# Performance work log

Measured on AMD Instinct MI355X. Metric: run time of the kernel, lower is better.

The kernel has to match this reference:

```python
import jax, jax.numpy as jnp
import numpy as np

# rho in the continualEP repo is the hard sigmoid: clamp to [0, 1]
def rho(x):
    return jnp.clip(x, 0.0, 1.0)

B = 16384
N0, N1, N2, ND = 10, 256, 256, 784  # size_tab = [N0, N1, N2, ND]; ns = 3
T_STEPS = 60


def _linear_init(key, out_dim, in_dim):
    s = 1.0 / np.sqrt(in_dim)
    return jax.random.uniform(key, (out_dim, in_dim), minval=-s, maxval=s, dtype=jnp.float32)


def setup_inputs() -> dict:
    key = jax.random.key(0)
    ks = jax.random.split(key, 8)
    data = jax.random.uniform(ks[0], (B, ND), dtype=jnp.float32)  # MNIST-like in [0,1]
    s0 = jnp.zeros((B, N0), jnp.float32)
    s1 = jnp.zeros((B, N1), jnp.float32)
    s2 = jnp.zeros((B, N2), jnp.float32)
    # w[0]: Linear(N1 -> N0, bias); w[1]: Linear(N0 -> N1, no bias), tied init W1 = W0^T
    W0 = _linear_init(ks[1], N0, N1)
    b0 = jax.random.uniform(ks[2], (N0,), minval=-1.0/np.sqrt(N1), maxval=1.0/np.sqrt(N1), dtype=jnp.float32)
    W1 = W0.T  # transpose-tied initialization (angle=0 branch)
    # w[2]: Linear(N2 -> N1, bias); w[3]: Linear(N1 -> N2, no bias), tied init W3 = W2^T
    W2 = _linear_init(ks[3], N1, N2)
    b2 = jax.random.uniform(ks[4], (N1,), minval=-1.0/np.sqrt(N2), maxval=1.0/np.sqrt(N2), dtype=jnp.float32)
    W3 = W2.T
    # w[4]: Linear(ND -> N2, bias)
    W4 = _linear_init(ks[5], N2, ND)
    b4 = jax.random.uniform(ks[6], (N2,), minval=-1.0/np.sqrt(ND), maxval=1.0/np.sqrt(ND), dtype=jnp.float32)
    return {"data": data, "s0": s0, "s1": s1, "s2": s2,
            "W0": W0, "b0": b0, "W1": W1, "W2": W2, "b2": b2,
            "W3": W3, "W4": W4, "b4": b4, "T": T_STEPS}


def reference(data, s0, s1, s2, W0, b0, W1, W2, b2, W3, W4, b4, T):
    """VFdisc.forward(method='nograd', beta=0): T sequential stepper() calls.

    stepper (dt=1):
      ds0 = -s0 + rho(W0 @ s1 + b0)
      ds1 = -s1 + rho(W2 @ s2 + b2 + W1 @ s0)
      ds2 = -s2 + rho(W4 @ data + b4 + W3 @ s1)
      s[i] <- s[i] + ds[i]   (all ds use the pre-update state)
    """
    # data drive is constant across steps; precompute it once
    drive = data @ W4.T + b4  # [B, N2]

    def step(carry, _):
        c0, c1, c2 = carry
        n0 = c0 + (-c0 + rho(c1 @ W0.T + b0))
        n1 = c1 + (-c1 + rho(c2 @ W2.T + b2 + c0 @ W1.T))
        n2 = c2 + (-c2 + rho(drive + c1 @ W3.T))
        return (n0, n1, n2), None

    (s0, s1, s2), _ = jax.lax.scan(step, (s0, s1, s2), None, length=T)
    return (s0, s1, s2)
```

## Files before the change

### kernel.cpp

```cpp
#include <hip/hip_runtime.h>

typedef __attribute__((ext_vector_type(8)))  short s8b;
typedef __attribute__((ext_vector_type(16))) float v16f;
typedef __attribute__((ext_vector_type(4)))  float v4f;
typedef __attribute__((ext_vector_type(4)))  unsigned int u32x4;
typedef __attribute__((ext_vector_type(4)))  int i32x4;
typedef __attribute__((ext_vector_type(16))) int i32x16;
typedef unsigned short u16;
typedef unsigned char u8;
typedef unsigned int u32;

#define Q25_ONE (1 << 25)

__device__ __forceinline__ void split1(float f, u16 &h, u16 &l) {
  unsigned u = __builtin_bit_cast(unsigned, f);
  unsigned hu = u & 0xffff0000u;
  float lf = f - __builtin_bit_cast(float, hu);
  h = (u16)(u >> 16);
  l = (u16)(__builtin_bit_cast(unsigned, lf) >> 16);
}

__device__ __forceinline__ v16f mfma32bf(s8b a, s8b b, v16f c) {
  return __builtin_amdgcn_mfma_f32_32x32x16_bf16(a, b, c, 0, 0, 0);
}
__device__ __forceinline__ i32x16 mfma_i8_32(i32x4 a, i32x4 b, i32x16 c) {
  return __builtin_amdgcn_mfma_i32_32x32x32_i8(a, b, c, 0, 0, 0);
}
__device__ __forceinline__ i32x4 mfma_i8_16(i32x4 a, i32x4 b, i32x4 c) {
  return __builtin_amdgcn_mfma_i32_16x16x64_i8(a, b, c, 0, 0, 0);
}

__device__ __forceinline__ u32 pack4(int b0, int b1, int b2, int b3) {
  u32 t0 = __builtin_amdgcn_perm((u32)b1, (u32)b0, 0x0C0C0400u);
  u32 t1 = __builtin_amdgcn_perm((u32)b3, (u32)b2, 0x0C0C0400u);
  return __builtin_amdgcn_perm(t1, t0, 0x05040100u);
}

__global__ void k_prep_w(const float* __restrict__ W2, const float* __restrict__ W3,
                         const float* __restrict__ W4, const float* __restrict__ W0,
                         signed char* __restrict__ w2q, signed char* __restrict__ w3q,
                         signed char* __restrict__ w0q,
                         u16* __restrict__ w4h, u16* __restrict__ w4l) {
  int i = blockIdx.x * 256 + threadIdx.x;
  if (i < 65536) {
    int q = (int)rintf(W2[i] * 2048.0f);
    q = min(max(q, -127), 127); w2q[i] = (signed char)q;
    q = (int)rintf(W3[i] * 2048.0f);
    q = min(max(q, -127), 127); w3q[i] = (signed char)q;
  }
  if (i < 4096) {
    int n = i >> 8, k = i & 255;
    float v = (n < 10) ? W0[n * 256 + k] : 0.0f;
    int q = (int)rintf(v * 2048.0f);
    q = min(max(q, -127), 127); w0q[i] = (signed char)q;
  }
  if (i < 200704) {
    u16 h, lo;
    split1(W4[i], h, lo); w4h[i] = h; w4l[i] = lo;
  }
}

__global__ void k_prep_small(const float* __restrict__ W1, const float* __restrict__ b0,
                             signed char* __restrict__ w1q, float* __restrict__ b0p) {
  int i = blockIdx.x * 256 + threadIdx.x;
  if (i < 8192) {
    int n = i >> 5, k = i & 31;
    float v = (k < 10) ? W1[n * 10 + k] : 0.0f;
    int q = (int)rintf(v * 2048.0f);
    q = min(max(q, -127), 127); w1q[i] = (signed char)q;
  } else if (i < 8208) {
    int k = i - 8192;
    b0p[k] = (k < 10) ? b0[k] : 0.0f;
  }
}

__device__ __forceinline__ void split_pack8(v4f x0, v4f x1, s8b &hi, s8b &lo) {
  float f[8];
  #pragma unroll
  for (int j = 0; j < 4; ++j) { f[j] = x0[j]; f[4 + j] = x1[j]; }
  u32x4 vh, vl;
  #pragma unroll
  for (int j = 0; j < 4; ++j) {
    unsigned u0 = __builtin_bit_cast(unsigned, f[2 * j]);
    unsigned u1 = __builtin_bit_cast(unsigned, f[2 * j + 1]);
    unsigned h0 = u0 & 0xffff0000u, h1 = u1 & 0xffff0000u;
    float l0 = f[2 * j]     - __builtin_bit_cast(float, h0);
    float l1 = f[2 * j + 1] - __builtin_bit_cast(float, h1);
    vh[j] = (u0 >> 16) | h1;
    vl[j] = (__builtin_bit_cast(unsigned, l0) >> 16) |
            (__builtin_bit_cast(unsigned, l1) & 0xffff0000u);
  }
  hi = __builtin_bit_cast(s8b, vh);
  lo = __builtin_bit_cast(s8b, vl);
}

__global__ void __launch_bounds__(256, 1) k_drive(
    const float* __restrict__ data, const u16* __restrict__ w4h,
    const u16* __restrict__ w4l, const float* __restrict__ b4,
    int* __restrict__ drive) {
  const int tid = threadIdx.x;
  const int w = tid >> 6, l = tid & 63;
  const int m = l & 31, g = l >> 5;
  const int rb = blockIdx.x * 64;
  const int nbase = w * 64;
  float b4v0 = b4[nbase + m], b4v1 = b4[nbase + 32 + m];
  v16f acc[2][2];
  #pragma unroll
  for (int r = 0; r < 16; ++r) {
    acc[0][0][r] = b4v0; acc[0][1][r] = b4v1;
    acc[1][0][r] = b4v0; acc[1][1][r] = b4v1;
  }
  for (int kt = 0; kt < 49; ++kt) {
    int k0 = kt * 16 + g * 8;
    s8b aH[2], aL[2], bH[2], bL[2];
    #pragma unroll
    for (int mt = 0; mt < 2; ++mt) {
      const float* p = data + (size_t)(rb + 32 * mt + m) * 784 + k0;
      v4f x0 = *(const v4f*)p;
      v4f x1 = *(const v4f*)(p + 4);
      split_pack8(x0, x1, aH[mt], aL[mt]);
    }
    #pragma unroll
    for (int nt = 0; nt < 2; ++nt) {
      int off = (nbase + 32 * nt + m) * 784 + k0;
      bH[nt] = *(const s8b*)(w4h + off);
      bL[nt] = *(const s8b*)(w4l + off);
    }
    #pragma unroll
    for (int mt = 0; mt < 2; ++mt)
      #pragma unroll
      for (int nt = 0; nt < 2; ++nt) {
        acc[mt][nt] = mfma32bf(aH[mt], bH[nt], acc[mt][nt]);
        acc[mt][nt] = mfma32bf(aL[mt], bH[nt], acc[mt][nt]);
        acc[mt][nt] = mfma32bf(aH[mt], bL[nt], acc[mt][nt]);
      }
  }
  #pragma unroll
  for (int mt = 0; mt < 2; ++mt)
    #pragma unroll
    for (int nt = 0; nt < 2; ++nt)
      #pragma unroll
      for (int r = 0; r < 16; ++r) {
        int row = rb + 32 * mt + (r & 3) + 8 * (r >> 2) + 4 * g;
        int col = nbase + 32 * nt + m;
        drive[(size_t)row * 256 + col] = (int)rintf(acc[mt][nt][r] * 33554432.0f);
      }
}

__global__ void __launch_bounds__(512, 2) k_main(
    const float* __restrict__ s0g, const float* __restrict__ s1g,
    const float* __restrict__ s2g, const float* __restrict__ b2,
    const int* __restrict__ Tp,
    const signed char* __restrict__ w2q, const signed char* __restrict__ w3q,
    const signed char* __restrict__ w0q, const signed char* __restrict__ w1q,
    const float* __restrict__ b0p, const int* __restrict__ drive,
    float* __restrict__ out0, float* __restrict__ out1, float* __restrict__ out2) {
  extern __shared__ u8 sm8[];
  u8* s1hA = sm8;
  u8* s1lA = sm8 + 8192;
  u8* s2hA = sm8 + 16384;
  u8* s2lA = sm8 + 24576;
  u8* s1hB = sm8 + 32768;
  u8* s1lB = sm8 + 40960;
  u8* s2hB = sm8 + 49152;
  u8* s2lB = sm8 + 57344;
  u8* s0hA = sm8 + 65536;
  u8* s0lA = sm8 + 67072;
  u8* s0hB = sm8 + 68608;
  u8* s0lB = sm8 + 70144;
  u8* w0s  = sm8 + 71680;

  const int tid = threadIdx.x;
  const int w = tid >> 6, l = tid & 63;
  const int m = l & 31, g = l >> 5;
  const int m16 = l & 15, g4 = l >> 4;
  const int rb = blockIdx.x * 32;

  i32x4 w2F[8], w3F[8], w1F;
  {
    const int wo = (w * 32 + m) * 256 + g * 16;
    #pragma unroll
    for (int kt = 0; kt < 8; ++kt) {
      w2F[kt] = *(const i32x4*)(w2q + wo + kt * 32);
      w3F[kt] = *(const i32x4*)(w3q + wo + kt * 32);
    }
    w1F = *(const i32x4*)(w1q + (w * 32 + m) * 32 + g * 16);
  }

  for (int i = tid; i < 8192; i += 512) {
    int row = i >> 8, c = i & 255;
    int idx = ((c >> 4) << 9) + row * 16 + (c & 15);
    int q = (int)rintf(s1g[(size_t)(rb + row) * 256 + c] * 16384.0f);
    int h = (q + 128) >> 8;
    s1hA[idx] = (u8)h; s1lA[idx] = (u8)(q - (h << 8));
    q = (int)rintf(s2g[(size_t)(rb + row) * 256 + c] * 16384.0f);
    h = (q + 128) >> 8;
    s2hA[idx] = (u8)h; s2lA[idx] = (u8)(q - (h << 8));
  }
  for (int i = tid; i < 1536; i += 512) {
    int row = i / 48, c = i - row * 48;
    float v = (c < 10) ? s0g[(rb + row) * 10 + c] : 0.0f;
    int q = (int)rintf(v * 16384.0f);
    int h = (q + 128) >> 8;
    s0hA[i] = (u8)h; s0lA[i] = (u8)(q - (h << 8));
    s0hB[i] = 0; s0lB[i] = 0;
  }
  if (tid < 256) {
    int r = tid >> 4, c = tid & 15;
    *(i32x4*)(w0s + c * 256 + r * 16) = *(const i32x4*)(w0q + r * 256 + c * 16);
  }

  int dr[16], b2r[16];
  {
    const int* drow = drive + (size_t)(rb + m) * 256 + w * 32 + 4 * g;
    const float* b2p = b2 + w * 32 + 4 * g;
    #pragma unroll
    for (int j = 0; j < 4; ++j) {
      i32x4 t = *(const i32x4*)(drow + 8 * j);
      #pragma unroll
      for (int e = 0; e < 4; ++e) {
        dr[j * 4 + e] = t[e];
        b2r[j * 4 + e] = (int)rintf(b2p[8 * j + e] * 33554432.0f);
      }
    }
  }
  int b0r[4];
  if (w < 2) {
    #pragma unroll
    for (int e = 0; e < 4; ++e)
      b0r[e] = (int)rintf(b0p[4 * g4 + e] * 33554432.0f);
  }

  const int T = Tp[0];
  const int rdB = m * 16 + g * 512;
  const int wrB = w * 1024 + m * 16 + 4 * g;
  const int rdB0 = (16 * w + m16) * 16 + g4 * 512;
  float* out1p = out1 + (size_t)(rb + m) * 256 + w * 32 + 4 * g;
  float* out2p = out2 + (size_t)(rb + m) * 256 + w * 32 + 4 * g;
  __syncthreads();

  u8 *s1ch = s1hA, *s1cl = s1lA, *s2ch = s2hA, *s2cl = s2lA;
  u8 *s1nh = s1hB, *s1nl = s1lB, *s2nh = s2hB, *s2nl = s2lB;
  u8 *s0ch = s0hA, *s0cl = s0lA, *s0nh = s0hB, *s0nl = s0lB;

  for (int t = 0; t < T; ++t) {
    const bool last = (t == T - 1);
    i32x16 hh, c1;

    #pragma unroll
    for (int r = 0; r < 16; ++r) { hh[r] = 0; c1[r] = 0; }
    {
      const u8* bh = s1ch + rdB;
      const u8* bl = s1cl + rdB;
      #pragma unroll
      for (int kt = 0; kt < 8; ++kt) {
        i32x4 Bh = *(const i32x4*)(bh + kt * 1024);
        i32x4 Bl = *(const i32x4*)(bl + kt * 1024);
        hh = mfma_i8_32(w3F[kt], Bh, hh);
        c1 = mfma_i8_32(w3F[kt], Bl, c1);
      }
    }
    #pragma unroll
    for (int j = 0; j < 4; ++j) {
      int hb[4], lb[4], cls[4];
      #pragma unroll
      for (int e = 0; e < 4; ++e) {
        int r = j * 4 + e;
        int pre = dr[r] + (hh[r] << 8) + c1[r];
        int cl = min(max(pre, 0), Q25_ONE);
        cls[e] = cl;
        int q14 = (cl + 1024) >> 11;
        int h = (cl + 263168) >> 19;
        hb[e] = h;
        lb[e] = q14 - (h << 8);
      }
      const int wo = wrB + ((j >> 1) << 9) + ((j & 1) << 3);
      *(u32*)(s2nh + wo) = pack4(hb[0], hb[1], hb[2], hb[3]);
      *(u32*)(s2nl + wo) = pack4(lb[0], lb[1], lb[2], lb[3]);
      if (last) {
        v4f ov;
        #pragma unroll
        for (int e = 0; e < 4; ++e) ov[e] = (float)cls[e] * 0x1p-25f;
        *(v4f*)(out2p + 8 * j) = ov;
      }
    }

    #pragma unroll
    for (int r = 0; r < 16; ++r) { hh[r] = 0; c1[r] = 0; }
    {
      i32x4 Bh = *(const i32x4*)(s0ch + m * 48 + g * 16);
      i32x4 Bl = *(const i32x4*)(s0cl + m * 48 + g * 16);
      hh = mfma_i8_32(w1F, Bh, hh);
      c1 = mfma_i8_32(w1F, Bl, c1);
    }
    {
      const u8* bh = s2ch + rdB;
      const u8* bl = s2cl + rdB;
      #pragma unroll
      for (int kt = 0; kt < 8; ++kt) {
        i32x4 Bh = *(const i32x4*)(bh + kt * 1024);
        i32x4 Bl = *(const i32x4*)(bl + kt * 1024);
        hh = mfma_i8_32(w2F[kt], Bh, hh);
        c1 = mfma_i8_32(w2F[kt], Bl, c1);
      }
    }
    #pragma unroll
    for (int j = 0; j < 4; ++j) {
      int hb[4], lb[4], cls[4];
      #pragma unroll
      for (int e = 0; e < 4; ++e) {
        int r = j * 4 + e;
        int pre = b2r[r] + (hh[r] << 8) + c1[r];
        int cl = min(max(pre, 0), Q25_ONE);
        cls[e] = cl;
        int q14 = (cl + 1024) >> 11;
        int h = (cl + 263168) >> 19;
        hb[e] = h;
        lb[e] = q14 - (h << 8);
      }
      const int wo = wrB + ((j >> 1) << 9) + ((j & 1) << 3);
      *(u32*)(s1nh + wo) = pack4(hb[0], hb[1], hb[2], hb[3]);
      *(u32*)(s1nl + wo) = pack4(lb[0], lb[1], lb[2], lb[3]);
      if (last) {
        v4f ov;
        #pragma unroll
        for (int e = 0; e < 4; ++e) ov[e] = (float)cls[e] * 0x1p-25f;
        *(v4f*)(out1p + 8 * j) = ov;
      }
    }

    if (w < 2) {
      const int arow = 16 * w + m16;
      const u8* bh = s1ch + rdB0;
      const u8* bl = s1cl + rdB0;
      i32x4 ph, p1;
      ph.x = ph.y = ph.z = ph.w = 0;
      p1.x = p1.y = p1.z = p1.w = 0;
      #pragma unroll
      for (int kt = 0; kt < 4; ++kt) {
        i32x4 Bh = *(const i32x4*)(bh + kt * 2048);
        i32x4 Bl = *(const i32x4*)(bl + kt * 2048);
        i32x4 aw = *(const i32x4*)(w0s + m16 * 16 + g4 * 256 + kt * 1024);
        ph = mfma_i8_16(aw, Bh, ph);
        p1 = mfma_i8_16(aw, Bl, p1);
      }
      int hb[4], lb[4], cls[4];
      #pragma unroll
      for (int e = 0; e < 4; ++e) {
        int pre = b0r[e] + (ph[e] << 8) + p1[e];
        int cl = min(max(pre, 0), Q25_ONE);
        cls[e] = cl;
        int q14 = (cl + 1024) >> 11;
        int h = (cl + 263168) >> 19;
        hb[e] = h;
        lb[e] = q14 - (h << 8);
      }
      u32 hq = pack4(hb[0], hb[1], hb[2], hb[3]);
      u32 lq = pack4(lb[0], lb[1], lb[2], lb[3]);
      if (g4 < 2) {
        *(u32*)(s0nh + arow * 48 + 4 * g4) = hq;
        *(u32*)(s0nl + arow * 48 + 4 * g4) = lq;
      } else if (g4 == 2) {
        *(u16*)(s0nh + arow * 48 + 8) = (u16)(hq & 0xffff);
        *(u16*)(s0nl + arow * 48 + 8) = (u16)(lq & 0xffff);
      }
      if (last) {
        #pragma unroll
        for (int e = 0; e < 4; ++e) {
          int n = 4 * g4 + e;
          if (n < 10) out0[(rb + arow) * 10 + n] = (float)cls[e] * 0x1p-25f;
        }
      }
    }

    __syncthreads();
    u8* tp;
    tp = s1ch; s1ch = s1nh; s1nh = tp;
    tp = s1cl; s1cl = s1nl; s1nl = tp;
    tp = s2ch; s2ch = s2nh; s2nh = tp;
    tp = s2cl; s2cl = s2nl; s2nl = tp;
    tp = s0ch; s0ch = s0nh; s0nh = tp;
    tp = s0cl; s0cl = s0nl; s0nl = tp;
  }
}

extern "C" void kernel_launch(void* const* d_in, const int* in_sizes, int n_in,
                              void* d_out, int out_size, void* d_ws, size_t ws_size,
                              hipStream_t stream) {
  const float* data = (const float*)d_in[0];
  const float* s0g  = (const float*)d_in[1];
  const float* s1g  = (const float*)d_in[2];
  const float* s2g  = (const float*)d_in[3];
  const float* W0   = (const float*)d_in[4];
  const float* b0   = (const float*)d_in[5];
  const float* W1   = (const float*)d_in[6];
  const float* W2   = (const float*)d_in[7];
  const float* b2   = (const float*)d_in[8];
  const float* W3   = (const float*)d_in[9];
  const float* W4   = (const float*)d_in[10];
  const float* b4   = (const float*)d_in[11];
  const int*   Tp   = (const int*)d_in[12];

  char* ws = (char*)d_ws;
  int* drive = (int*)ws;
  size_t off = 16777216;
  signed char* w2q = (signed char*)(ws + off); off += 65536;
  signed char* w3q = (signed char*)(ws + off); off += 65536;
  signed char* w0q = (signed char*)(ws + off); off += 4096;
  signed char* w1q = (signed char*)(ws + off); off += 8192;
  u16* w4h = (u16*)(ws + off); off += 401408;
  u16* w4l = (u16*)(ws + off); off += 401408;
  float* b0p = (float*)(ws + off); off += 64;

  float* out0 = (float*)d_out;
  float* out1 = out0 + 16384 * 10;
  float* out2 = out1 + 16384 * 256;

  hipFuncSetAttribute((const void*)k_main,
                      hipFuncAttributeMaxDynamicSharedMemorySize, 75776);

  k_prep_w<<<784, 256, 0, stream>>>(W2, W3, W4, W0, w2q, w3q, w0q, w4h, w4l);
  k_prep_small<<<33, 256, 0, stream>>>(W1, b0, w1q, b0p);
  k_drive<<<256, 256, 0, stream>>>(data, w4h, w4l, b4, drive);
  k_main<<<512, 512, 75776, stream>>>(s0g, s1g, s2g, b2, Tp,
      w2q, w3q, w0q, w1q, b0p, drive, out0, out1, out2);
}
```

Measured before the change: 340.1 us.

## Single-buffer state in LDS with register staging and two barriers per step

Drops the double-buffered shared-memory state so each step computes all new s0/s1/s2 values into registers, then writes them back after a barrier, followed by a second barrier. This roughly halves LDS use per block (75776 to 38912 bytes), which may allow more blocks per CU. It also folds the bias and drive terms into the MFMA accumulator init and narrows the s0 row stride to 32 bytes. In exchange it adds a second __syncthreads per step and extra live registers for the staged packed values.

```diff
diff --git a/kernel.cpp b/kernel.cpp
--- a/kernel.cpp
+++ b/kernel.cpp
@@ -156,19 +156,13 @@
     const float* __restrict__ b0p, const int* __restrict__ drive,
     float* __restrict__ out0, float* __restrict__ out1, float* __restrict__ out2) {
   extern __shared__ u8 sm8[];
-  u8* s1hA = sm8;
-  u8* s1lA = sm8 + 8192;
-  u8* s2hA = sm8 + 16384;
-  u8* s2lA = sm8 + 24576;
-  u8* s1hB = sm8 + 32768;
-  u8* s1lB = sm8 + 40960;
-  u8* s2hB = sm8 + 49152;
-  u8* s2lB = sm8 + 57344;
-  u8* s0hA = sm8 + 65536;
-  u8* s0lA = sm8 + 67072;
-  u8* s0hB = sm8 + 68608;
-  u8* s0lB = sm8 + 70144;
-  u8* w0s  = sm8 + 71680;
+  u8* s1h = sm8;
+  u8* s1l = sm8 + 8192;
+  u8* s2h = sm8 + 16384;
+  u8* s2l = sm8 + 24576;
+  u8* s0h = sm8 + 32768;
+  u8* s0l = sm8 + 33792;
+  u8* w0s = sm8 + 34816;
 
   const int tid = threadIdx.x;
   const int w = tid >> 6, l = tid & 63;
@@ -192,18 +186,17 @@
     int idx = ((c >> 4) << 9) + row * 16 + (c & 15);
     int q = (int)rintf(s1g[(size_t)(rb + row) * 256 + c] * 16384.0f);
     int h = (q + 128) >> 8;
-    s1hA[idx] = (u8)h; s1lA[idx] = (u8)(q - (h << 8));
+    s1h[idx] = (u8)h; s1l[idx] = (u8)(q - (h << 8));
     q = (int)rintf(s2g[(size_t)(rb + row) * 256 + c] * 16384.0f);
     h = (q + 128) >> 8;
-    s2hA[idx] = (u8)h; s2lA[idx] = (u8)(q - (h << 8));
-  }
-  for (int i = tid; i < 1536; i += 512) {
-    int row = i / 48, c = i - row * 48;
+    s2h[idx] = (u8)h; s2l[idx] = (u8)(q - (h << 8));
+  }
+  for (int i = tid; i < 1024; i += 512) {
+    int row = i >> 5, c = i & 31;
     float v = (c < 10) ? s0g[(rb + row) * 10 + c] : 0.0f;
     int q = (int)rintf(v * 16384.0f);
     int h = (q + 128) >> 8;
-    s0hA[i] = (u8)h; s0lA[i] = (u8)(q - (h << 8));
-    s0hB[i] = 0; s0lB[i] = 0;
+    s0h[i] = (u8)h; s0l[i] = (u8)(q - (h << 8));
   }
   if (tid < 256) {
     int r = tid >> 4, c = tid & 15;
@@ -239,25 +232,26 @@
   float* out2p = out2 + (size_t)(rb + m) * 256 + w * 32 + 4 * g;
   __syncthreads();
 
-  u8 *s1ch = s1hA, *s1cl = s1lA, *s2ch = s2hA, *s2cl = s2lA;
-  u8 *s1nh = s1hB, *s1nl = s1lB, *s2nh = s2hB, *s2nl = s2lB;
-  u8 *s0ch = s0hA, *s0cl = s0lA, *s0nh = s0hB, *s0nl = s0lB;
-
   for (int t = 0; t < T; ++t) {
     const bool last = (t == T - 1);
+    u32 n1h[4], n1l[4], n2h[4], n2l[4], n0h, n0l;
     i32x16 hh, c1;
 
     #pragma unroll
-    for (int r = 0; r < 16; ++r) { hh[r] = 0; c1[r] = 0; }
+    for (int r = 0; r < 16; ++r) { hh[r] = 0; c1[r] = b2r[r]; }
     {
-      const u8* bh = s1ch + rdB;
-      const u8* bl = s1cl + rdB;
+      i32x4 Bh = *(const i32x4*)(s0h + m * 32 + g * 16);
+      i32x4 Bl = *(const i32x4*)(s0l + m * 32 + g * 16);
+      hh = mfma_i8_32(w1F, Bh, hh);
+      c1 = mfma_i8_32(w1F, Bl, c1);
+      const u8* bh = s2h + rdB;
+      const u8* bl = s2l + rdB;
       #pragma unroll
       for (int kt = 0; kt < 8; ++kt) {
-        i32x4 Bh = *(const i32x4*)(bh + kt * 1024);
-        i32x4 Bl = *(const i32x4*)(bl + kt * 1024);
-        hh = mfma_i8_32(w3F[kt], Bh, hh);
-        c1 = mfma_i8_32(w3F[kt], Bl, c1);
+        i32x4 B2h = *(const i32x4*)(bh + kt * 1024);
+        i32x4 B2l = *(const i32x4*)(bl + kt * 1024);
+        hh = mfma_i8_32(w2F[kt], B2h, hh);
+        c1 = mfma_i8_32(w2F[kt], B2l, c1);
       }
     }
     #pragma unroll
@@ -266,7 +260,7 @@
       #pragma unroll
       for (int e = 0; e < 4; ++e) {
         int r = j * 4 + e;
-        int pre = dr[r] + (hh[r] << 8) + c1[r];
+        int pre = (hh[r] << 8) + c1[r];
         int cl = min(max(pre, 0), Q25_ONE);
         cls[e] = cl;
         int q14 = (cl + 1024) >> 11;
@@ -274,53 +268,8 @@
         hb[e] = h;
         lb[e] = q14 - (h << 8);
       }
-      const int wo = wrB + ((j >> 1) << 9) + ((j & 1) << 3);
-      *(u32*)(s2nh + wo) = pack4(hb[0], hb[1], hb[2], hb[3]);
-      *(u32*)(s2nl + wo) = pack4(lb[0], lb[1], lb[2], lb[3]);
-      if (last) {
-        v4f ov;
-        #pragma unroll
-        for (int e = 0; e < 4; ++e) ov[e] = (float)cls[e] * 0x1p-25f;
-        *(v4f*)(out2p + 8 * j) = ov;
-      }
-    }
-
-    #pragma unroll
-    for (int r = 0; r < 16; ++r) { hh[r] = 0; c1[r] = 0; }
-    {
-      i32x4 Bh = *(const i32x4*)(s0ch + m * 48 + g * 16);
-      i32x4 Bl = *(const i32x4*)(s0cl + m * 48 + g * 16);
-      hh = mfma_i8_32(w1F, Bh, hh);
-      c1 = mfma_i8_32(w1F, Bl, c1);
-    }
-    {
-      const u8* bh = s2ch + rdB;
-      const u8* bl = s2cl + rdB;
-      #pragma unroll
-      for (int kt = 0; kt < 8; ++kt) {
-        i32x4 Bh = *(const i32x4*)(bh + kt * 1024);
-        i32x4 Bl = *(const i32x4*)(bl + kt * 1024);
-        hh = mfma_i8_32(w2F[kt], Bh, hh);
-        c1 = mfma_i8_32(w2F[kt], Bl, c1);
-      }
-    }
-    #pragma unroll
-    for (int j = 0; j < 4; ++j) {
-      int hb[4], lb[4], cls[4];
-      #pragma unroll
-      for (int e = 0; e < 4; ++e) {
-        int r = j * 4 + e;
-        int pre = b2r[r] + (hh[r] << 8) + c1[r];
-        int cl = min(max(pre, 0), Q25_ONE);
-        cls[e] = cl;
-        int q14 = (cl + 1024) >> 11;
-        int h = (cl + 263168) >> 19;
-        hb[e] = h;
-        lb[e] = q14 - (h << 8);
-      }
-      const int wo = wrB + ((j >> 1) << 9) + ((j & 1) << 3);
-      *(u32*)(s1nh + wo) = pack4(hb[0], hb[1], hb[2], hb[3]);
-      *(u32*)(s1nl + wo) = pack4(lb[0], lb[1], lb[2], lb[3]);
+      n1h[j] = pack4(hb[0], hb[1], hb[2], hb[3]);
+      n1l[j] = pack4(lb[0], lb[1], lb[2], lb[3]);
       if (last) {
         v4f ov;
         #pragma unroll
@@ -330,9 +279,8 @@
     }
 
     if (w < 2) {
-      const int arow = 16 * w + m16;
-      const u8* bh = s1ch + rdB0;
-      const u8* bl = s1cl + rdB0;
+      const u8* bh = s1h + rdB0;
+      const u8* bl = s1l + rdB0;
       i32x4 ph, p1;
       ph.x = ph.y = ph.z = ph.w = 0;
       p1.x = p1.y = p1.z = p1.w = 0;
@@ -355,32 +303,75 @@
         hb[e] = h;
         lb[e] = q14 - (h << 8);
       }
-      u32 hq = pack4(hb[0], hb[1], hb[2], hb[3]);
-      u32 lq = pack4(lb[0], lb[1], lb[2], lb[3]);
-      if (g4 < 2) {
-        *(u32*)(s0nh + arow * 48 + 4 * g4) = hq;
-        *(u32*)(s0nl + arow * 48 + 4 * g4) = lq;
-      } else if (g4 == 2) {
-        *(u16*)(s0nh + arow * 48 + 8) = (u16)(hq & 0xffff);
-        *(u16*)(s0nl + arow * 48 + 8) = (u16)(lq & 0xffff);
-      }
+      n0h = pack4(hb[0], hb[1], hb[2], hb[3]);
+      n0l = pack4(lb[0], lb[1], lb[2], lb[3]);
       if (last) {
         #pragma unroll
         for (int e = 0; e < 4; ++e) {
           int n = 4 * g4 + e;
-          if (n < 10) out0[(rb + arow) * 10 + n] = (float)cls[e] * 0x1p-25f;
+          if (n < 10) out0[(rb + 16 * w + m16) * 10 + n] = (float)cls[e] * 0x1p-25f;
         }
       }
     }
 
+    #pragma unroll
+    for (int r = 0; r < 16; ++r) { hh[r] = 0; c1[r] = dr[r]; }
+    {
+      const u8* bh = s1h + rdB;
+      const u8* bl = s1l + rdB;
+      #pragma unroll
+      for (int kt = 0; kt < 8; ++kt) {
+        i32x4 Bh = *(const i32x4*)(bh + kt * 1024);
+        i32x4 Bl = *(const i32x4*)(bl + kt * 1024);
+        hh = mfma_i8_32(w3F[kt], Bh, hh);
+        c1 = mfma_i8_32(w3F[kt], Bl, c1);
+      }
+    }
+    #pragma unroll
+    for (int j = 0; j < 4; ++j) {
+      int hb[4], lb[4], cls[4];
+      #pragma unroll
+      for (int e = 0; e < 4; ++e) {
+        int r = j * 4 + e;
+        int pre = (hh[r] << 8) + c1[r];
+        int cl = min(max(pre, 0), Q25_ONE);
+        cls[e] = cl;
+        int q14 = (cl + 1024) >> 11;
+        int h = (cl + 263168) >> 19;
+        hb[e] = h;
+        lb[e] = q14 - (h << 8);
+      }
+      n2h[j] = pack4(hb[0], hb[1], hb[2], hb[3]);
+      n2l[j] = pack4(lb[0], lb[1], lb[2], lb[3]);
+      if (last) {
+        v4f ov;
+        #pragma unroll
+        for (int e = 0; e < 4; ++e) ov[e] = (float)cls[e] * 0x1p-25f;
+        *(v4f*)(out2p + 8 * j) = ov;
+      }
+    }
+
     __syncthreads();
-    u8* tp;
-    tp = s1ch; s1ch = s1nh; s1nh = tp;
-    tp = s1cl; s1cl = s1nl; s1nl = tp;
-    tp = s2ch; s2ch = s2nh; s2nh = tp;
-    tp = s2cl; s2cl = s2nl; s2nl = tp;
-    tp = s0ch; s0ch = s0nh; s0nh = tp;
-    tp = s0cl; s0cl = s0nl; s0nl = tp;
+
+    #pragma unroll
+    for (int j = 0; j < 4; ++j) {
+      const int wo = wrB + ((j >> 1) << 9) + ((j & 1) << 3);
+      *(u32*)(s1h + wo) = n1h[j];
+      *(u32*)(s1l + wo) = n1l[j];
+      *(u32*)(s2h + wo) = n2h[j];
+      *(u32*)(s2l + wo) = n2l[j];
+    }
+    if (w < 2) {
+      const int arow = 16 * w + m16;
+      if (g4 < 2) {
+        *(u32*)(s0h + arow * 32 + 4 * g4) = n0h;
+        *(u32*)(s0l + arow * 32 + 4 * g4) = n0l;
+      } else if (g4 == 2) {
+        *(u16*)(s0h + arow * 32 + 8) = (u16)(n0h & 0xffff);
+        *(u16*)(s0l + arow * 32 + 8) = (u16)(n0l & 0xffff);
+      }
+    }
+    __syncthreads();
   }
 }
 
@@ -417,11 +408,11 @@
   float* out2 = out1 + 16384 * 256;
 
   hipFuncSetAttribute((const void*)k_main,
-                      hipFuncAttributeMaxDynamicSharedMemorySize, 75776);
+                      hipFuncAttributeMaxDynamicSharedMemorySize, 38912);
 
   k_prep_w<<<784, 256, 0, stream>>>(W2, W3, W4, W0, w2q, w3q, w0q, w4h, w4l);
   k_prep_small<<<33, 256, 0, stream>>>(W1, b0, w1q, b0p);
   k_drive<<<256, 256, 0, stream>>>(data, w4h, w4l, b4, drive);
-  k_main<<<512, 512, 75776, stream>>>(s0g, s1g, s2g, b2, Tp,
+  k_main<<<512, 512, 38912, stream>>>(s0g, s1g, s2g, b2, Tp,
       w2q, w3q, w0q, w1q, b0p, drive, out0, out1, out2);
 }
```

After: 361.3 us. 6.2% more time.
